# Kernel tuning notes

Measured on AMD Instinct MI355X. Metric: run time of the kernel, lower is better.

The kernel has to match this reference:

```python
import jax, jax.numpy as jnp
import numpy as np

N = 100000      # nodes
E = 3200000     # edges
G = 512         # graphs
F = 12          # num_features
NHID = 64
HGCN = NHID - 3   # 61, GCNConv output dim
EMB_OUT = 64 - F + 2  # 54


def _p(key, shape, scale):
    return jax.random.normal(key, shape, jnp.float32) * scale


def setup_inputs() -> dict:
    key = jax.random.key(0)
    ks = jax.random.split(key, 24)
    inp = {}
    inp["x"] = jax.random.normal(ks[0], (N, F), jnp.float32)
    inp["edge_index"] = jax.random.randint(ks[1], (2, E), 0, N)
    inp["batch"] = jnp.sort(jax.random.randint(ks[2], (N,), 0, G))
    inp["known_mask"] = jax.random.randint(ks[3], (E // 3,), 0, E)
    inp["unk_mask"] = jax.random.randint(ks[4], (E // 3,), 0, E)
    inp["obs_mask"] = jax.random.randint(ks[5], (E // 3,), 0, E)
    inp["fn_averages"] = jax.random.normal(ks[6], (G, 2), jnp.float32)
    inp["infection_rates"] = jax.random.normal(ks[7], (G, 1), jnp.float32)
    # parameters
    inp["msg_weights"] = jax.random.normal(ks[8], (3,), jnp.float32)
    inp["W_emb"] = _p(ks[9], (2, EMB_OUT), 0.5)
    inp["b_emb"] = jnp.zeros((EMB_OUT,), jnp.float32)
    inp["W_gcn"] = _p(ks[10], (64, HGCN), 0.125)
    inp["b_gcn"] = jnp.zeros((HGCN,), jnp.float32)
    inp["W_fn1"] = _p(ks[11], (3, 16), 0.5)
    inp["b_fn1"] = jnp.zeros((16,), jnp.float32)
    inp["W_fn2"] = _p(ks[12], (16, 3), 0.25)
    inp["b_fn2"] = jnp.zeros((3,), jnp.float32)
    inp["W_bb1"] = _p(ks[13], (NHID, NHID), 0.125)
    inp["b_bb1"] = jnp.zeros((NHID,), jnp.float32)
    inp["W_out"] = _p(ks[14], (NHID, 1), 0.125)
    inp["b_out"] = jnp.zeros((1,), jnp.float32)
    return inp


def reference(x, edge_index, batch, known_mask, unk_mask, obs_mask,
              fn_averages, infection_rates, msg_weights,
              W_emb, b_emb, W_gcn, b_gcn, W_fn1, b_fn1, W_fn2, b_fn2,
              W_bb1, b_bb1, W_out, b_out):
    gelu = lambda t: jax.nn.gelu(t, approximate=False)
    n = x.shape[0]
    e = edge_index.shape[1]
    g = fn_averages.shape[0]

    sp = jax.nn.softmax(msg_weights)
    ew = jnp.ones((e,), x.dtype)
    ew = ew.at[known_mask].set(sp[0]).at[unk_mask].set(sp[1]).at[obs_mask].set(sp[2])

    # node embedding: Linear on first 2 feats, concat rest -> (N, 64)
    h = jnp.concatenate([x[:, :2] @ W_emb + b_emb, x[:, 2:]], axis=1)

    # GCNConv(64 -> 61) with edge weights and self-loops
    h = h @ W_gcn                                  # (N, HGCN) transform first
    row, col = edge_index[0], edge_index[1]
    loop = jnp.arange(n)
    row_f = jnp.concatenate([row, loop])
    col_f = jnp.concatenate([col, loop])
    ew_f = jnp.concatenate([ew, jnp.ones((n,), ew.dtype)])
    deg = jax.ops.segment_sum(ew_f, col_f, num_segments=n)   # weighted in-degree
    dis = jnp.where(deg > 0, jax.lax.rsqrt(jnp.maximum(deg, 1e-12)), 0.0)
    norm = dis[row_f] * ew_f * dis[col_f]                    # (E+N,)
    out = jax.ops.segment_sum(norm[:, None] * h[row_f], col_f, num_segments=n)
    out = gelu(out + b_gcn)                                  # dropout = identity (eval)

    # global_add_pool over graphs
    pooled = jax.ops.segment_sum(out, batch, num_segments=g)  # (G, HGCN)

    # fn embeddings MLP on (fn_averages, infection_rate)
    extra = jnp.concatenate([fn_averages.reshape(-1, 2),
                             infection_rates.reshape(-1, 1)], axis=1)  # (G, 3)
    fn_e = gelu(extra @ W_fn1 + b_fn1) @ W_fn2 + b_fn2        # (G, 3)

    z = jnp.concatenate([pooled, fn_e], axis=1)               # (G, NHID)
    z = gelu(z @ W_bb1 + b_bb1)
    logits = z @ W_out + b_out                                # (G, 1)
    return logits
```

## Files before the change

kernel.cpp:

```cpp
#include <hip/hip_runtime.h>
#include <hip/hip_fp16.h>
#include <math.h>

#define F_IN 12
#define NHID 64
#define HGCN 61
#define EMB_OUT 54
#define SCAN_CH 1024
#define PART_R 8192
#define DEG_SCALE 32768.0f
#define W_SCALE 16384.0f

typedef unsigned int uint;
typedef unsigned short ushort;
typedef unsigned char uchar;

__device__ __forceinline__ float gelu_exact(float v) {
    return 0.5f * v * (1.0f + erff(v * 0.70710678118654752440f));
}

__device__ __forceinline__ void atomic_add_f32(float* p, float v) {
    unsafeAtomicAdd(p, v);
}

__global__ __launch_bounds__(256) void k1_hist_prep(
        const int* __restrict__ ei, uint* __restrict__ H, uchar* __restrict__ wclass,
        const float* __restrict__ msg_w, const float* __restrict__ W_emb,
        const float* __restrict__ b_emb, const float* __restrict__ W_gcn,
        uint* __restrict__ spq, uint* __restrict__ sq15,
        float* __restrict__ W_eff, float* __restrict__ b_eff,
        int E, int NB, int NBLK) {
    __shared__ uint hist[512];
    __shared__ float ssp[4];
    int blk = blockIdx.x, t = threadIdx.x;
    hist[t] = 0; hist[t + 256] = 0;
    if (blk == 0 && t == 0) {
        float m = fmaxf(msg_w[0], fmaxf(msg_w[1], msg_w[2]));
        float e0 = expf(msg_w[0] - m), e1 = expf(msg_w[1] - m), e2 = expf(msg_w[2] - m);
        float s = e0 + e1 + e2;
        ssp[0] = 1.0f; ssp[1] = e0 / s; ssp[2] = e1 / s; ssp[3] = e2 / s;
    }
    __syncthreads();
    if (blk == 0) {
        if (t < 4) {
            spq[t]  = __float2uint_rn(ssp[t] * DEG_SCALE);
            sq15[t] = __float2uint_rn(ssp[t] * W_SCALE);
        }
        if (t < HGCN) {
            float be = 0.f, w0 = 0.f, w1 = 0.f;
            for (int k = 0; k < EMB_OUT; ++k) {
                float g = W_gcn[k * HGCN + t];
                be += b_emb[k] * g;
                w0 += W_emb[k] * g;
                w1 += W_emb[EMB_OUT + k] * g;
            }
            b_eff[t] = be;
            W_eff[0 * 64 + t] = w0;
            W_eff[1 * 64 + t] = w1;
            for (int f = 2; f < F_IN; ++f)
                W_eff[f * 64 + t] = W_gcn[(EMB_OUT + f - 2) * HGCN + t];
        }
    }
    int lo = blk * PART_R, hi = min(lo + PART_R, E);
    for (int i = lo + t; i < hi; i += 256) {
        wclass[i] = 0;
        atomicAdd(&hist[((uint)ei[E + i]) >> 8], 1u);
    }
    __syncthreads();
    for (int b = t; b < NB; b += 256) H[(size_t)b * NBLK + blk] = hist[b];
}

__global__ void set_mask_u8(uchar* __restrict__ wclass, const int* __restrict__ mask,
                            uchar v, int n) {
    int i = blockIdx.x * blockDim.x + threadIdx.x;
    if (i < n) wclass[mask[i]] = v;
}

__global__ void scan_partial_kernel(const int* __restrict__ cnt, int* __restrict__ startv,
                                    int* __restrict__ bsum, int n) {
    __shared__ int s[256];
    int t = threadIdx.x;
    int base = blockIdx.x * SCAN_CH + t * 4;
    int v0 = (base + 0 < n) ? cnt[base + 0] : 0;
    int v1 = (base + 1 < n) ? cnt[base + 1] : 0;
    int v2 = (base + 2 < n) ? cnt[base + 2] : 0;
    int v3 = (base + 3 < n) ? cnt[base + 3] : 0;
    int loc = v0 + v1 + v2 + v3;
    s[t] = loc;
    __syncthreads();
    for (int off = 1; off < 256; off <<= 1) {
        int u = (t >= off) ? s[t - off] : 0;
        __syncthreads();
        s[t] += u;
        __syncthreads();
    }
    int ex = s[t] - loc;
    if (t == 255) bsum[blockIdx.x] = s[255];
    if (base + 0 < n) startv[base + 0] = ex;
    if (base + 1 < n) startv[base + 1] = ex + v0;
    if (base + 2 < n) startv[base + 2] = ex + v0 + v1;
    if (base + 3 < n) startv[base + 3] = ex + v0 + v1 + v2;
}

__global__ void scan_add_kernel(int* __restrict__ startv, const int* __restrict__ bsum, int n) {
    __shared__ int soff;
    int b = blockIdx.x;
    if (threadIdx.x == 0) {
        int q = (b * 256) / SCAN_CH;
        int acc = 0;
        for (int j = 0; j < q; ++j) acc += bsum[j];
        soff = acc;
    }
    __syncthreads();
    int i = b * 256 + threadIdx.x;
    if (i < n) startv[i] += soff;
}

__global__ __launch_bounds__(256) void k3_partition(
        const int* __restrict__ ei, const uchar* __restrict__ wclass,
        const uint* __restrict__ H, const uint* __restrict__ Hs,
        uint* __restrict__ recSorted, int E, int NB, int NBLK) {
    __shared__ uint recs[PART_R];
    __shared__ ushort sbkt[PART_R];
    __shared__ uint scanA[512];
    __shared__ uint scanB[512];
    __shared__ int  gbase[512];
    __shared__ uint cursor[512];
    int blk = blockIdx.x, t = threadIdx.x;
    int lo = blk * PART_R, hi = min(lo + PART_R, E);
    int cntTot = hi - lo;
    uint h0 = (t < NB)       ? H[(size_t)t * NBLK + blk]         : 0u;
    uint h1 = (t + 256 < NB) ? H[(size_t)(t + 256) * NBLK + blk] : 0u;
    uint* src = scanA; uint* dst = scanB;
    src[t] = h0; src[t + 256] = h1;
    __syncthreads();
    for (int off = 1; off < 512; off <<= 1) {
        dst[t]       = src[t]       + ((t >= off)       ? src[t - off]       : 0u);
        dst[t + 256] = src[t + 256] + ((t + 256 >= off) ? src[t + 256 - off] : 0u);
        __syncthreads();
        uint* tmp = src; src = dst; dst = tmp;
    }
    uint l0 = (t == 0) ? 0u : src[t - 1];
    uint l1 = src[t + 255];
    cursor[t] = l0; cursor[t + 256] = l1;
    if (t < NB)       gbase[t]       = (int)Hs[(size_t)t * NBLK + blk]         - (int)l0;
    if (t + 256 < NB) gbase[t + 256] = (int)Hs[(size_t)(t + 256) * NBLK + blk] - (int)l1;
    __syncthreads();
    for (int i = lo + t; i < hi; i += 256) {
        uint row = (uint)ei[i];
        uint col = (uint)ei[E + i];
        uint b = col >> 8;
        uint rec = (row << 10) | ((col & 255u) << 2) | (uint)wclass[i];
        uint slot = atomicAdd(&cursor[b], 1u);
        recs[slot] = rec;
        sbkt[slot] = (ushort)b;
    }
    __syncthreads();
    for (int s = t; s < cntTot; s += 256)
        recSorted[gbase[sbkt[s]] + s] = recs[s];
}

__global__ __launch_bounds__(256) void k2k4(
        const uint* __restrict__ recSorted, const uint* __restrict__ Hs,
        const uint* __restrict__ spq, const uint* __restrict__ sq15,
        uint* __restrict__ cnt, uint* __restrict__ startv, float* __restrict__ dis,
        uint* __restrict__ payload, int E, int NB, int NBLK, int n_nodes) {
    __shared__ uint hcnt[256], hdeg[256], sA[256], sB[256];
    __shared__ uint cur[256];
    __shared__ uint sq[4], wq[4];
    int b = blockIdx.x, t = threadIdx.x;
    hcnt[t] = 0; hdeg[t] = 0;
    if (t < 4) { sq[t] = spq[t]; wq[t] = sq15[t]; }
    __syncthreads();
    uint lo = Hs[(size_t)b * NBLK];
    uint hi = (b + 1 < NB) ? Hs[(size_t)(b + 1) * NBLK] : (uint)E;
    for (uint i = lo + t; i < hi; i += 256) {
        uint r = recSorted[i];
        atomicAdd(&hcnt[(r >> 2) & 255u], 1u);
        atomicAdd(&hdeg[(r >> 2) & 255u], sq[r & 3u]);
    }
    __syncthreads();
    uint* src = sA; uint* dst = sB;
    src[t] = hcnt[t];
    __syncthreads();
    for (int off = 1; off < 256; off <<= 1) {
        dst[t] = src[t] + ((t >= off) ? src[t - off] : 0u);
        __syncthreads();
        uint* tmp = src; src = dst; dst = tmp;
    }
    uint excl = (t == 0) ? 0u : src[t - 1];
    int node = (b << 8) + t;
    if (node < n_nodes) {
        cnt[node] = hcnt[t];
        startv[node] = lo + excl;
        float deg = (float)hdeg[t] * (1.0f / DEG_SCALE) + 1.0f;
        dis[node] = rsqrtf(deg);
    }
    cur[t] = lo + excl;
    __syncthreads();
    for (uint i = lo + t; i < hi; i += 256) {
        uint r = recSorted[i];
        uint pos = atomicAdd(&cur[(r >> 2) & 255u], 1u);
        payload[pos] = ((r >> 10) << 15) | wq[r & 3u];
    }
}

__global__ void h2_kernel(const float* __restrict__ x, const float* __restrict__ W_eff,
                          const float* __restrict__ b_eff, const float* __restrict__ dis,
                          __half* __restrict__ h2, float* __restrict__ pooled, int g64,
                          int n_nodes) {
    int gid = blockIdx.x * 256 + threadIdx.x;
    if (gid < g64) pooled[gid] = 0.0f;
    int node = blockIdx.x * 4 + (threadIdx.x >> 6);
    int d = threadIdx.x & 63;
    if (node >= n_nodes) return;
    float v = 0.f;
    if (d < HGCN) {
        v = b_eff[d];
#pragma unroll
        for (int f = 0; f < F_IN; ++f)
            v += x[node * F_IN + f] * W_eff[f * 64 + d];
        v *= dis[node];
    }
    h2[node * 64 + d] = __float2half(v);
}

__global__ void gather_pool_kernel(const uint* __restrict__ payload,
                                   const uint* __restrict__ startv, const uint* __restrict__ cnt,
                                   const float* __restrict__ dis,
                                   const __half2* __restrict__ h2v,
                                   const float* __restrict__ b_gcn, const int* __restrict__ batch,
                                   float* __restrict__ pooled, int n_nodes) {
    int node = blockIdx.x * 4 + (threadIdx.x >> 6);
    int lane = threadIdx.x & 63;
    int g = lane >> 5;
    int sub = lane & 31;
    if (node >= n_nodes) return;
    int s = (int)startv[node];
    int m = (int)cnt[node];
    const float inv = 1.0f / W_SCALE;
    float accx = 0.f, accy = 0.f;
    if (g == 0) {
        float2 hv = __half22float2(h2v[node * 32 + sub]);
        accx = hv.x;
        accy = hv.y;
    }
    for (int j0 = 0; j0 < m; j0 += 64) {
        uint p = 0;
        if (j0 + lane < m) p = payload[s + j0 + lane];
        int lim = min(64, m - j0);
        int npairs = (lim + 1) >> 1;
        int k = 0;
        for (; k + 8 <= npairs; k += 8) {
            uint p0 = __shfl(p, 2 * (k + 0) + g);
            uint p1 = __shfl(p, 2 * (k + 1) + g);
            uint p2 = __shfl(p, 2 * (k + 2) + g);
            uint p3 = __shfl(p, 2 * (k + 3) + g);
            uint p4 = __shfl(p, 2 * (k + 4) + g);
            uint p5 = __shfl(p, 2 * (k + 5) + g);
            uint p6 = __shfl(p, 2 * (k + 6) + g);
            uint p7 = __shfl(p, 2 * (k + 7) + g);
            float2 h0 = __half22float2(h2v[(p0 >> 15) * 32 + sub]);
            float2 h1 = __half22float2(h2v[(p1 >> 15) * 32 + sub]);
            float2 h2f = __half22float2(h2v[(p2 >> 15) * 32 + sub]);
            float2 h3 = __half22float2(h2v[(p3 >> 15) * 32 + sub]);
            float2 h4 = __half22float2(h2v[(p4 >> 15) * 32 + sub]);
            float2 h5 = __half22float2(h2v[(p5 >> 15) * 32 + sub]);
            float2 h6 = __half22float2(h2v[(p6 >> 15) * 32 + sub]);
            float2 h7 = __half22float2(h2v[(p7 >> 15) * 32 + sub]);
            float w0 = (float)(p0 & 32767u) * inv;
            float w1 = (float)(p1 & 32767u) * inv;
            float w2 = (float)(p2 & 32767u) * inv;
            float w3 = (float)(p3 & 32767u) * inv;
            float w4 = (float)(p4 & 32767u) * inv;
            float w5 = (float)(p5 & 32767u) * inv;
            float w6 = (float)(p6 & 32767u) * inv;
            float w7 = (float)(p7 & 32767u) * inv;
            accx += w0 * h0.x; accy += w0 * h0.y;
            accx += w1 * h1.x; accy += w1 * h1.y;
            accx += w2 * h2f.x; accy += w2 * h2f.y;
            accx += w3 * h3.x; accy += w3 * h3.y;
            accx += w4 * h4.x; accy += w4 * h4.y;
            accx += w5 * h5.x; accy += w5 * h5.y;
            accx += w6 * h6.x; accy += w6 * h6.y;
            accx += w7 * h7.x; accy += w7 * h7.y;
        }
        for (; k < npairs; ++k) {
            uint pk = __shfl(p, 2 * k + g);
            float2 hk = __half22float2(h2v[(pk >> 15) * 32 + sub]);
            float wk = (float)(pk & 32767u) * inv;
            accx += wk * hk.x; accy += wk * hk.y;
        }
    }
    accx += __shfl_xor(accx, 32);
    accy += __shfl_xor(accy, 32);
    int d = 2 * sub + g;
    float val = (g ? accy : accx) * dis[node];
    if (d < HGCN) {
        float v = gelu_exact(val + b_gcn[d]);
        atomic_add_f32(&pooled[batch[node] * 64 + d], v);
    }
}

__global__ void final_kernel(const float* __restrict__ pooled,
                             const float* __restrict__ fn_avg,
                             const float* __restrict__ inf_rate,
                             const float* __restrict__ W_fn1, const float* __restrict__ b_fn1,
                             const float* __restrict__ W_fn2, const float* __restrict__ b_fn2,
                             const float* __restrict__ W_bb1, const float* __restrict__ b_bb1,
                             const float* __restrict__ W_out, const float* __restrict__ b_out,
                             float* __restrict__ logits) {
    __shared__ float z[64];
    __shared__ float t1[16];
    int g = blockIdx.x;
    int t = threadIdx.x;
    if (t < HGCN) z[t] = pooled[g * 64 + t];
    float e0 = fn_avg[g * 2], e1 = fn_avg[g * 2 + 1], e2 = inf_rate[g];
    if (t < 16) {
        float a = e0 * W_fn1[t] + e1 * W_fn1[16 + t] + e2 * W_fn1[32 + t] + b_fn1[t];
        t1[t] = gelu_exact(a);
    }
    __syncthreads();
    if (t < 3) {
        float a = b_fn2[t];
#pragma unroll
        for (int k = 0; k < 16; ++k) a += t1[k] * W_fn2[k * 3 + t];
        z[HGCN + t] = a;
    }
    __syncthreads();
    float acc = b_bb1[t];
#pragma unroll 8
    for (int k = 0; k < 64; ++k) acc += z[k] * W_bb1[k * 64 + t];
    float p = gelu_exact(acc) * W_out[t];
#pragma unroll
    for (int off = 32; off > 0; off >>= 1) p += __shfl_down(p, off);
    if (t == 0) logits[g] = p + b_out[0];
}

extern "C" void kernel_launch(void* const* d_in, const int* in_sizes, int n_in,
                              void* d_out, int out_size, void* d_ws, size_t ws_size,
                              hipStream_t stream) {
    const float* x        = (const float*)d_in[0];
    const int*   ei       = (const int*)d_in[1];
    const int*   batch    = (const int*)d_in[2];
    const int*   known    = (const int*)d_in[3];
    const int*   unk      = (const int*)d_in[4];
    const int*   obs      = (const int*)d_in[5];
    const float* fn_avg   = (const float*)d_in[6];
    const float* inf_rate = (const float*)d_in[7];
    const float* msg_w    = (const float*)d_in[8];
    const float* W_emb    = (const float*)d_in[9];
    const float* b_emb    = (const float*)d_in[10];
    const float* W_gcn    = (const float*)d_in[11];
    const float* b_gcn    = (const float*)d_in[12];
    const float* W_fn1    = (const float*)d_in[13];
    const float* b_fn1    = (const float*)d_in[14];
    const float* W_fn2    = (const float*)d_in[15];
    const float* b_fn2    = (const float*)d_in[16];
    const float* W_bb1    = (const float*)d_in[17];
    const float* b_bb1    = (const float*)d_in[18];
    const float* W_out    = (const float*)d_in[19];
    const float* b_out    = (const float*)d_in[20];
    float* logits = (float*)d_out;

    const int n_nodes = in_sizes[0] / F_IN;
    const int E       = in_sizes[1] / 2;
    const int nk = in_sizes[3], nu = in_sizes[4], no = in_sizes[5];
    const int G = in_sizes[6] / 2;

    const int NB   = (n_nodes + 255) >> 8;
    const int NBLK = (E + PART_R - 1) / PART_R;
    const int L    = NB * NBLK;
    const int nbL  = (L + SCAN_CH - 1) / SCAN_CH;

    char* ws = (char*)d_ws;
    size_t off = 0;
    auto alloc = [&](size_t bytes) -> void* {
        void* p = ws + off;
        off += (bytes + 255) & ~size_t(255);
        return p;
    };
    uchar*  wclass    = (uchar*)alloc(sizeof(uchar) * (size_t)E);
    uint*   recSorted = (uint*)alloc(sizeof(uint) * (size_t)E);
    uint*   H         = (uint*)alloc(sizeof(uint) * (size_t)L);
    uint*   Hs        = (uint*)alloc(sizeof(uint) * (size_t)L);
    int*    bsum      = (int*)alloc(sizeof(int) * (size_t)(nbL + 1));
    __half* h2        = (__half*)alloc(sizeof(__half) * (size_t)n_nodes * 64);
    uint*   payload   = (uint*)alloc(sizeof(uint) * (size_t)E);
    uint*   cntv      = (uint*)alloc(sizeof(uint) * (size_t)n_nodes);
    uint*   startv    = (uint*)alloc(sizeof(uint) * (size_t)n_nodes);
    float*  dis       = (float*)alloc(sizeof(float) * (size_t)n_nodes);
    float*  pooled    = (float*)alloc(sizeof(float) * (size_t)G * 64);
    float*  W_eff     = (float*)alloc(sizeof(float) * F_IN * 64);
    float*  b_eff     = (float*)alloc(sizeof(float) * 64);
    uint*   spq       = (uint*)alloc(sizeof(uint) * 4);
    uint*   sq15      = (uint*)alloc(sizeof(uint) * 4);

    k1_hist_prep<<<NBLK, 256, 0, stream>>>(ei, H, wclass, msg_w, W_emb, b_emb, W_gcn,
                                           spq, sq15, W_eff, b_eff, E, NB, NBLK);
    set_mask_u8<<<(nk + 255) / 256, 256, 0, stream>>>(wclass, known, 1, nk);
    set_mask_u8<<<(nu + 255) / 256, 256, 0, stream>>>(wclass, unk, 2, nu);
    set_mask_u8<<<(no + 255) / 256, 256, 0, stream>>>(wclass, obs, 3, no);
    scan_partial_kernel<<<nbL, 256, 0, stream>>>((const int*)H, (int*)Hs, bsum, L);
    scan_add_kernel<<<(L + 255) / 256, 256, 0, stream>>>((int*)Hs, bsum, L);
    k3_partition<<<NBLK, 256, 0, stream>>>(ei, wclass, H, Hs, recSorted, E, NB, NBLK);
    k2k4<<<NB, 256, 0, stream>>>(recSorted, Hs, spq, sq15, cntv, startv, dis, payload,
                                 E, NB, NBLK, n_nodes);
    h2_kernel<<<(n_nodes + 3) / 4, 256, 0, stream>>>(x, W_eff, b_eff, dis, h2, pooled,
                                                     G * 64, n_nodes);
    gather_pool_kernel<<<(n_nodes + 3) / 4, 256, 0, stream>>>(payload, startv, cntv, dis,
                                                              (const __half2*)h2, b_gcn, batch,
                                                              pooled, n_nodes);
    final_kernel<<<G, 64, 0, stream>>>(pooled, fn_avg, inf_rate, W_fn1, b_fn1,
                                       W_fn2, b_fn2, W_bb1, b_bb1, W_out, b_out, logits);
}
```

Measured before the change: 216.4 us.

## Split feature gather into two half-width passes over separate fp16 tables

Stores the per-node fp16 features as two separate 32-wide tables (low and high halves) and runs the edge gather twice, once per half. Each pass handles four edges at a time with 16 lanes per edge row, so it gathers 64-byte rows from a table half the size of the original. The aim is to make each pass's random-access working set (about 6.4 MB) fit better in cache. The cost is reading the payload and CSR metadata twice, an extra kernel launch, and an added cross-lane reduction.

```diff
diff --git a/kernel.cpp b/kernel.cpp
--- a/kernel.cpp
+++ b/kernel.cpp
@@ -207,8 +207,8 @@
 
 __global__ void h2_kernel(const float* __restrict__ x, const float* __restrict__ W_eff,
                           const float* __restrict__ b_eff, const float* __restrict__ dis,
-                          __half* __restrict__ h2, float* __restrict__ pooled, int g64,
-                          int n_nodes) {
+                          __half* __restrict__ h2lo, __half* __restrict__ h2hi,
+                          float* __restrict__ pooled, int g64, int n_nodes) {
     int gid = blockIdx.x * 256 + threadIdx.x;
     if (gid < g64) pooled[gid] = 0.0f;
     int node = blockIdx.x * 4 + (threadIdx.x >> 6);
@@ -222,82 +222,78 @@
             v += x[node * F_IN + f] * W_eff[f * 64 + d];
         v *= dis[node];
     }
-    h2[node * 64 + d] = __float2half(v);
-}
-
-__global__ void gather_pool_kernel(const uint* __restrict__ payload,
+    if (d < 32) h2lo[node * 32 + d] = __float2half(v);
+    else        h2hi[node * 32 + (d - 32)] = __float2half(v);
+}
+
+template <int PASS>
+__global__ void gather_half_kernel(const uint* __restrict__ payload,
                                    const uint* __restrict__ startv, const uint* __restrict__ cnt,
                                    const float* __restrict__ dis,
-                                   const __half2* __restrict__ h2v,
+                                   const uint* __restrict__ h2h,
                                    const float* __restrict__ b_gcn, const int* __restrict__ batch,
                                    float* __restrict__ pooled, int n_nodes) {
     int node = blockIdx.x * 4 + (threadIdx.x >> 6);
     int lane = threadIdx.x & 63;
-    int g = lane >> 5;
-    int sub = lane & 31;
+    int g4  = lane >> 4;
+    int s16 = lane & 15;
     if (node >= n_nodes) return;
     int s = (int)startv[node];
     int m = (int)cnt[node];
     const float inv = 1.0f / W_SCALE;
-    float accx = 0.f, accy = 0.f;
-    if (g == 0) {
-        float2 hv = __half22float2(h2v[node * 32 + sub]);
-        accx = hv.x;
-        accy = hv.y;
+    float a0 = 0.f, a1 = 0.f;
+    if (g4 == 0) {
+        uint q = h2h[node * 16 + s16];
+        float2 hv = __half22float2(*(const __half2*)&q);
+        a0 = hv.x; a1 = hv.y;
     }
     for (int j0 = 0; j0 < m; j0 += 64) {
         uint p = 0;
         if (j0 + lane < m) p = payload[s + j0 + lane];
         int lim = min(64, m - j0);
-        int npairs = (lim + 1) >> 1;
+        int nq = (lim + 3) >> 2;
         int k = 0;
-        for (; k + 8 <= npairs; k += 8) {
-            uint p0 = __shfl(p, 2 * (k + 0) + g);
-            uint p1 = __shfl(p, 2 * (k + 1) + g);
-            uint p2 = __shfl(p, 2 * (k + 2) + g);
-            uint p3 = __shfl(p, 2 * (k + 3) + g);
-            uint p4 = __shfl(p, 2 * (k + 4) + g);
-            uint p5 = __shfl(p, 2 * (k + 5) + g);
-            uint p6 = __shfl(p, 2 * (k + 6) + g);
-            uint p7 = __shfl(p, 2 * (k + 7) + g);
-            float2 h0 = __half22float2(h2v[(p0 >> 15) * 32 + sub]);
-            float2 h1 = __half22float2(h2v[(p1 >> 15) * 32 + sub]);
-            float2 h2f = __half22float2(h2v[(p2 >> 15) * 32 + sub]);
-            float2 h3 = __half22float2(h2v[(p3 >> 15) * 32 + sub]);
-            float2 h4 = __half22float2(h2v[(p4 >> 15) * 32 + sub]);
-            float2 h5 = __half22float2(h2v[(p5 >> 15) * 32 + sub]);
-            float2 h6 = __half22float2(h2v[(p6 >> 15) * 32 + sub]);
-            float2 h7 = __half22float2(h2v[(p7 >> 15) * 32 + sub]);
-            float w0 = (float)(p0 & 32767u) * inv;
-            float w1 = (float)(p1 & 32767u) * inv;
-            float w2 = (float)(p2 & 32767u) * inv;
-            float w3 = (float)(p3 & 32767u) * inv;
-            float w4 = (float)(p4 & 32767u) * inv;
-            float w5 = (float)(p5 & 32767u) * inv;
-            float w6 = (float)(p6 & 32767u) * inv;
-            float w7 = (float)(p7 & 32767u) * inv;
-            accx += w0 * h0.x; accy += w0 * h0.y;
-            accx += w1 * h1.x; accy += w1 * h1.y;
-            accx += w2 * h2f.x; accy += w2 * h2f.y;
-            accx += w3 * h3.x; accy += w3 * h3.y;
-            accx += w4 * h4.x; accy += w4 * h4.y;
-            accx += w5 * h5.x; accy += w5 * h5.y;
-            accx += w6 * h6.x; accy += w6 * h6.y;
-            accx += w7 * h7.x; accy += w7 * h7.y;
+        for (; k + 8 <= nq; k += 8) {
+            uint p0 = __shfl(p, 4 * (k + 0) + g4);
+            uint p1 = __shfl(p, 4 * (k + 1) + g4);
+            uint p2 = __shfl(p, 4 * (k + 2) + g4);
+            uint p3 = __shfl(p, 4 * (k + 3) + g4);
+            uint p4 = __shfl(p, 4 * (k + 4) + g4);
+            uint p5 = __shfl(p, 4 * (k + 5) + g4);
+            uint p6 = __shfl(p, 4 * (k + 6) + g4);
+            uint p7 = __shfl(p, 4 * (k + 7) + g4);
+            uint q0 = h2h[(p0 >> 15) * 16 + s16];
+            uint q1 = h2h[(p1 >> 15) * 16 + s16];
+            uint q2 = h2h[(p2 >> 15) * 16 + s16];
+            uint q3 = h2h[(p3 >> 15) * 16 + s16];
+            uint q4 = h2h[(p4 >> 15) * 16 + s16];
+            uint q5 = h2h[(p5 >> 15) * 16 + s16];
+            uint q6 = h2h[(p6 >> 15) * 16 + s16];
+            uint q7 = h2h[(p7 >> 15) * 16 + s16];
+#define ACC(pi, qi)                                                        \
+            {                                                              \
+                float w = (float)(pi & 32767u) * inv;                      \
+                float2 hv = __half22float2(*(const __half2*)&qi);          \
+                a0 += w * hv.x; a1 += w * hv.y;                            \
+            }
+            ACC(p0, q0) ACC(p1, q1) ACC(p2, q2) ACC(p3, q3)
+            ACC(p4, q4) ACC(p5, q5) ACC(p6, q6) ACC(p7, q7)
         }
-        for (; k < npairs; ++k) {
-            uint pk = __shfl(p, 2 * k + g);
-            float2 hk = __half22float2(h2v[(pk >> 15) * 32 + sub]);
-            float wk = (float)(pk & 32767u) * inv;
-            accx += wk * hk.x; accy += wk * hk.y;
+        for (; k < nq; ++k) {
+            uint pk = __shfl(p, 4 * k + g4);
+            uint qk = h2h[(pk >> 15) * 16 + s16];
+            ACC(pk, qk)
         }
-    }
-    accx += __shfl_xor(accx, 32);
-    accy += __shfl_xor(accy, 32);
-    int d = 2 * sub + g;
-    float val = (g ? accy : accx) * dis[node];
-    if (d < HGCN) {
-        float v = gelu_exact(val + b_gcn[d]);
+#undef ACC
+    }
+    a0 += __shfl_xor(a0, 16); a0 += __shfl_xor(a0, 32);
+    a1 += __shfl_xor(a1, 16); a1 += __shfl_xor(a1, 32);
+    float b0 = __shfl(a0, lane >> 1);
+    float b1 = __shfl(a1, lane >> 1);
+    float val = (lane & 1) ? b1 : b0;
+    int d = PASS * 32 + lane;
+    if (lane < 32 && d < HGCN) {
+        float v = gelu_exact(val * dis[node] + b_gcn[d]);
         atomic_add_f32(&pooled[batch[node] * 64 + d], v);
     }
 }
@@ -385,7 +381,8 @@
     uint*   H         = (uint*)alloc(sizeof(uint) * (size_t)L);
     uint*   Hs        = (uint*)alloc(sizeof(uint) * (size_t)L);
     int*    bsum      = (int*)alloc(sizeof(int) * (size_t)(nbL + 1));
-    __half* h2        = (__half*)alloc(sizeof(__half) * (size_t)n_nodes * 64);
+    __half* h2lo      = (__half*)alloc(sizeof(__half) * (size_t)n_nodes * 32);
+    __half* h2hi      = (__half*)alloc(sizeof(__half) * (size_t)n_nodes * 32);
     uint*   payload   = (uint*)alloc(sizeof(uint) * (size_t)E);
     uint*   cntv      = (uint*)alloc(sizeof(uint) * (size_t)n_nodes);
     uint*   startv    = (uint*)alloc(sizeof(uint) * (size_t)n_nodes);
@@ -406,11 +403,14 @@
     k3_partition<<<NBLK, 256, 0, stream>>>(ei, wclass, H, Hs, recSorted, E, NB, NBLK);
     k2k4<<<NB, 256, 0, stream>>>(recSorted, Hs, spq, sq15, cntv, startv, dis, payload,
                                  E, NB, NBLK, n_nodes);
-    h2_kernel<<<(n_nodes + 3) / 4, 256, 0, stream>>>(x, W_eff, b_eff, dis, h2, pooled,
-                                                     G * 64, n_nodes);
-    gather_pool_kernel<<<(n_nodes + 3) / 4, 256, 0, stream>>>(payload, startv, cntv, dis,
-                                                              (const __half2*)h2, b_gcn, batch,
-                                                              pooled, n_nodes);
+    h2_kernel<<<(n_nodes + 3) / 4, 256, 0, stream>>>(x, W_eff, b_eff, dis, h2lo, h2hi,
+                                                     pooled, G * 64, n_nodes);
+    gather_half_kernel<0><<<(n_nodes + 3) / 4, 256, 0, stream>>>(payload, startv, cntv, dis,
+                                                                 (const uint*)h2lo, b_gcn, batch,
+                                                                 pooled, n_nodes);
+    gather_half_kernel<1><<<(n_nodes + 3) / 4, 256, 0, stream>>>(payload, startv, cntv, dis,
+                                                                 (const uint*)h2hi, b_gcn, batch,
+                                                                 pooled, n_nodes);
     final_kernel<<<G, 64, 0, stream>>>(pooled, fn_avg, inf_rate, W_fn1, b_fn1,
                                        W_fn2, b_fn2, W_bb1, b_bb1, W_out, b_out, logits);
 }
```

After: 254.5 us. 17.6% more time.
